# Optimization experiments

Measured on AMD Instinct MI355X. Metric: run time of the kernel, lower is better.

Reference implementation:

```python
import jax, jax.numpy as jnp
import numpy as np

B, S, D, H = 4, 2048, 512, 8
DH = D // H  # 64


def setup_inputs() -> dict:
    key = jax.random.key(0)
    ks = jax.random.split(key, 12)
    sc = 0.02
    return {
        "embed": jax.random.normal(ks[0], (B, S, D), dtype=jnp.float32),
        "Wq": jax.random.normal(ks[1], (H, DH, D), dtype=jnp.float32) * sc,
        "bq": jax.random.normal(ks[2], (H, DH), dtype=jnp.float32) * sc,
        "Wk": jax.random.normal(ks[3], (H, DH, D), dtype=jnp.float32) * sc,
        "bk": jax.random.normal(ks[4], (H, DH), dtype=jnp.float32) * sc,
        "Wv": jax.random.normal(ks[5], (H, DH, D), dtype=jnp.float32) * sc,
        "bv": jax.random.normal(ks[6], (H, DH), dtype=jnp.float32) * sc,
        "Wo": jax.random.normal(ks[7], (D, D), dtype=jnp.float32) * sc,
        "bo": jax.random.normal(ks[8], (D,), dtype=jnp.float32) * sc,
        "gamma": jnp.ones((D,), dtype=jnp.float32),
        "beta": jnp.zeros((D,), dtype=jnp.float32),
    }


def reference(embed, Wq, bq, Wk, bk, Wv, bv, Wo, bo, gamma, beta):
    # Per-head linear projections, vectorized over heads: [B,H,S,DH]
    q = jnp.einsum("bsd,hed->bhse", embed, Wq) + bq[None, :, None, :]
    k = jnp.einsum("bsd,hed->bhse", embed, Wk) + bk[None, :, None, :]
    v = jnp.einsum("bsd,hed->bhse", embed, Wv) + bv[None, :, None, :]

    # Full score matrix [B,H,S,S], tril applied to RAW scores (zeros, not -inf),
    # scaled by sqrt(embedding_dim) -- faithful to the original module's math.
    att = jnp.einsum("bhse,bhte->bhst", q, k)
    att = jnp.tril(att)
    att = att / jnp.sqrt(jnp.float32(D))
    att = jax.nn.softmax(att, axis=-1)

    out = jnp.einsum("bhst,bhte->bhse", att, v)  # [B,H,S,DH]
    # concat heads along feature dim -> [B,S,D]
    out = jnp.transpose(out, (0, 2, 1, 3)).reshape(B, S, D)

    x = out @ Wo.T + bo
    x = x + embed

    # LayerNorm over last dim
    mu = jnp.mean(x, axis=-1, keepdims=True)
    var = jnp.var(x, axis=-1, keepdims=True)
    x = (x - mu) / jnp.sqrt(var + 1e-5) * gamma + beta
    return x
```

## Files before the change

### kernel.cpp

```cpp
#include <hip/hip_runtime.h>
#include <hip/hip_bf16.h>


typedef __bf16 bf16;
typedef __bf16 bf16x8 __attribute__((ext_vector_type(8)));
typedef __bf16 bf16x4v __attribute__((ext_vector_type(4)));
typedef float f32x4 __attribute__((ext_vector_type(4)));

#define S_LEN 2048
#define DMODEL 512
#define QSCALE 0.06375870914f

#define GLDS(g, l) __builtin_amdgcn_global_load_lds(                  \
    (const __attribute__((address_space(1))) void*)(g),               \
    (__attribute__((address_space(3))) void*)(l), 16, 0, 0)

#define EXP2(x) __builtin_amdgcn_exp2f(x)

__global__ __launch_bounds__(256) void cast_all(
    const float* __restrict__ embed, const float* __restrict__ Wq,
    const float* __restrict__ Wk, const float* __restrict__ Wv,
    const float* __restrict__ Wo,
    bf16* __restrict__ Eb, bf16* __restrict__ Wqkv, bf16* __restrict__ Wob) {
  int i = blockIdx.x * 256 + threadIdx.x;
  const float* src;
  bf16* dst;
  int il;
  if (i < 1048576) {
    src = embed; dst = Eb; il = i;
  } else {
    int j = i - 1048576;
    int w = j >> 16;
    il = j & 65535;
    src = (w == 0) ? Wq : (w == 1) ? Wk : (w == 2) ? Wv : Wo;
    dst = (w == 3) ? Wob : Wqkv + (size_t)w * 262144;
  }
  float4 v = reinterpret_cast<const float4*>(src)[il];
  bf16x4v o;
  o[0] = (bf16)v.x; o[1] = (bf16)v.y; o[2] = (bf16)v.z; o[3] = (bf16)v.w;
  *reinterpret_cast<bf16x4v*>(dst + (size_t)il * 4) = o;
}

__device__ __forceinline__ void gemm128_core(
    const bf16* __restrict__ A, const bf16* __restrict__ Bw,
    int row0, int col0, bf16* As, bf16* Bs, f32x4 (&acc)[4][4]) {
  int tid = threadIdx.x;
  int w = tid >> 6, l = tid & 63, lr = l & 15, lg = l >> 4;
  int wr = w >> 1, wc = w & 1;

  int srow = w * 8 + (l >> 3);
  int scol = ((l & 7) ^ (srow & 7)) << 3;
  const bf16* ga = A + (size_t)(row0 + srow) * DMODEL + scol;
  const bf16* gb = Bw + (size_t)(col0 + srow) * DMODEL + scol;
  char* asb = (char*)As;
  char* bsb = (char*)Bs;
  int sbase = w * 1024;

  int aoff[4], boff[4];
#pragma unroll
  for (int m = 0; m < 4; ++m) {
    aoff[m] = (wr * 64 + m * 16 + lr) * 128 + (((lg ^ (lr & 7))) << 4);
    boff[m] = (wc * 64 + m * 16 + lr) * 128 + (((lg ^ (lr & 7))) << 4);
  }

  for (int k0 = 0; k0 < DMODEL; k0 += 64) {
#pragma unroll
    for (int qt = 0; qt < 4; ++qt) {
      GLDS(ga + (size_t)qt * 32 * DMODEL, asb + qt * 4096 + sbase);
      GLDS(gb + (size_t)qt * 32 * DMODEL, bsb + qt * 4096 + sbase);
    }
    ga += 64; gb += 64;
    __syncthreads();

    bf16x8 af[2][4], bfv[2][4];
#pragma unroll
    for (int m = 0; m < 4; ++m) {
      af[0][m] = *(const bf16x8*)(asb + aoff[m]);
      af[1][m] = *(const bf16x8*)(asb + (aoff[m] ^ 0x40));
      bfv[0][m] = *(const bf16x8*)(bsb + boff[m]);
      bfv[1][m] = *(const bf16x8*)(bsb + (boff[m] ^ 0x40));
    }
#pragma unroll
    for (int m = 0; m < 4; ++m)
#pragma unroll
      for (int n = 0; n < 4; ++n) {
        acc[m][n] = __builtin_amdgcn_mfma_f32_16x16x32_bf16(af[0][m], bfv[0][n], acc[m][n], 0, 0, 0);
        acc[m][n] = __builtin_amdgcn_mfma_f32_16x16x32_bf16(af[1][m], bfv[1][n], acc[m][n], 0, 0, 0);
      }
    __syncthreads();
  }
}

__global__ __launch_bounds__(256) void gemm_qkv(
    const bf16* __restrict__ A, const bf16* __restrict__ Wqkv,
    const float* __restrict__ bq, const float* __restrict__ bk, const float* __restrict__ bv,
    bf16* __restrict__ Qb, bf16* __restrict__ Kb, bf16* __restrict__ Vt) {
  __shared__ __align__(16) bf16 As[128 * 64];
  __shared__ __align__(16) bf16 Bs[128 * 64];
  int row0 = blockIdx.x * 128, col0 = blockIdx.y * 128;
  f32x4 acc[4][4] = {};
  gemm128_core(A, Wqkv, row0, col0, As, Bs, acc);

  int tid = threadIdx.x;
  int w = tid >> 6, l = tid & 63, lr = l & 15, lg = l >> 4;
  int wr = w >> 1, wc = w & 1;
  int z2 = col0 >> 9;
  if (z2 < 2) {
    bf16* O = z2 ? Kb : Qb;
    const float* bias = z2 ? bk : bq;
    float qs = z2 ? 1.0f : QSCALE;
#pragma unroll
    for (int n = 0; n < 4; ++n) {
      int cg = (col0 & 511) + wc * 64 + n * 16 + lr;
      float bi = bias[cg];
#pragma unroll
      for (int m = 0; m < 4; ++m) {
        int rg = row0 + wr * 64 + m * 16 + lg * 4;
#pragma unroll
        for (int r = 0; r < 4; ++r)
          O[(size_t)(rg + r) * DMODEL + cg] = (bf16)((acc[m][n][r] + bi) * qs);
      }
    }
  } else {
#pragma unroll
    for (int n = 0; n < 4; ++n) {
      int ep = (col0 & 511) + wc * 64 + n * 16 + lr;
      int h = ep >> 6, e = ep & 63;
      float bi = bv[ep];
#pragma unroll
      for (int m = 0; m < 4; ++m) {
        int rg = row0 + wr * 64 + m * 16 + lg * 4;
        int b = rg >> 11, s0 = rg & 2047;
        bf16x4v pk;
#pragma unroll
        for (int r = 0; r < 4; ++r) pk[r] = (bf16)(acc[m][n][r] + bi);
        *(bf16x4v*)(Vt + ((size_t)((b * 8 + h) * 64 + e)) * S_LEN + s0) = pk;
      }
    }
  }
}

__global__ __launch_bounds__(256) void gemm_wo(
    const bf16* __restrict__ A, const bf16* __restrict__ W,
    const float* __restrict__ bo, const float* __restrict__ embed,
    bf16* __restrict__ X) {
  __shared__ __align__(16) bf16 As[128 * 64];
  __shared__ __align__(16) bf16 Bs[128 * 64];
  int row0 = blockIdx.x * 128, col0 = blockIdx.y * 128;
  f32x4 acc[4][4] = {};
  gemm128_core(A, W, row0, col0, As, Bs, acc);

  int tid = threadIdx.x;
  int w = tid >> 6, l = tid & 63, lr = l & 15, lg = l >> 4;
  int wr = w >> 1, wc = w & 1;
#pragma unroll
  for (int n = 0; n < 4; ++n) {
    int cg = col0 + wc * 64 + n * 16 + lr;
    float bi = bo[cg];
#pragma unroll
    for (int m = 0; m < 4; ++m) {
      int rg = row0 + wr * 64 + m * 16 + lg * 4;
#pragma unroll
      for (int r = 0; r < 4; ++r)
        X[(size_t)(rg + r) * DMODEL + cg] =
            (bf16)(acc[m][n][r] + bi + embed[(size_t)(rg + r) * DMODEL + cg]);
    }
  }
}

__global__ __launch_bounds__(256) void suf_kernel(const bf16* __restrict__ Vt,
                                                  float* __restrict__ SUF) {
  int bh = blockIdx.x >> 3;
  int eg = blockIdx.x & 7;
  int el = threadIdx.x & 7;
  int seg = threadIdx.x >> 3;
  int e = eg * 8 + el;
  __shared__ float segtot[32][9];
  const bf16* vrow = Vt + ((size_t)bh * 64 + e) * S_LEN;
  float loc[4];
  float carry = 0.f;
#pragma unroll
  for (int j = 3; j >= 0; --j) {
    int jj = seg * 4 + j;
    bf16x8 a = *(const bf16x8*)(vrow + jj * 16);
    bf16x8 b2 = *(const bf16x8*)(vrow + jj * 16 + 8);
    float s = 0.f;
#pragma unroll
    for (int k = 0; k < 8; ++k) s += (float)a[k] + (float)b2[k];
    carry += s;
    loc[j] = carry;
  }
  segtot[seg][el] = carry;
  __syncthreads();
  float add = 0.f;
  for (int s2 = seg + 1; s2 < 32; ++s2) add += segtot[s2][el];
  float* srow = SUF + (size_t)bh * 129 * 64 + e;
#pragma unroll
  for (int j = 0; j < 4; ++j) srow[(size_t)(seg * 4 + j) * 64] = loc[j] + add;
  if (seg == 0) srow[(size_t)128 * 64] = 0.f;
}

__global__ __launch_bounds__(512) void flash_attn(
    const bf16* __restrict__ Qb, const bf16* __restrict__ Kb,
    const bf16* __restrict__ Vt, const float* __restrict__ SUF,
    bf16* __restrict__ attO) {
  int id = blockIdx.x;
  int g = id & 7;
  int j = id >> 3;
  int bh = g * 4 + (j & 3);
  int p = 15 - (j >> 2);
  int b = bh >> 3, h = bh & 7;
  int tid = threadIdx.x;
  int w = tid >> 6, l = tid & 63, lr = l & 15, lg = l >> 4;
  int wsub = w & 3;
  int qtile = (w < 4) ? (16 + p) : (15 - p);
  int qb = qtile * 64;
  int qbw = qb + 16 * wsub;
  int tmax_w = qbw + 16;
  int nt = (18 + p) >> 1;
  int ntw = (tmax_w + 127) >> 7;

  __shared__ __align__(16) bf16 kl[2][128 * 64];
  __shared__ __align__(16) bf16 vl[2][2][64 * 64];
  __shared__ __align__(16) bf16 pl[8][16 * 64];

  const bf16* qptr = Qb + ((size_t)(b * S_LEN) + qbw + lr) * DMODEL + h * 64 + lg * 8;
  bf16x8 aq0 = *(const bf16x8*)(qptr);
  bf16x8 aq1 = *(const bf16x8*)(qptr + 32);

  float lsum[4] = {0.f, 0.f, 0.f, 0.f};
  f32x4 acc[4] = {};

  int grow = tid >> 3, gch = tid & 7;
  int sch = ((gch ^ (grow & 7)) << 3);
  const bf16* Kg = Kb + ((size_t)(b * S_LEN) + grow) * DMODEL + h * 64 + sch;
  const bf16* Vg = Vt + ((size_t)(bh * 64) + grow) * S_LEN + sch;
  int sdst = w * 1024;

  int sw0 = (lg ^ (lr & 7)) << 4;
  int sw4 = sw0 ^ 0x40;
  char* plb = (char*)pl[w];

  GLDS(Kg, (char*)kl[0] + sdst);
  GLDS(Kg + (size_t)64 * DMODEL, (char*)kl[0] + 8192 + sdst);
  GLDS(Vg, (char*)vl[0][0] + sdst);
  GLDS(Vg + 64, (char*)vl[0][1] + sdst);
  asm volatile("s_waitcnt vmcnt(0)" ::: "memory");
  __syncthreads();

  int cur = 0;
  for (int it = 0; it < nt; ++it) {
    int t0 = it << 7;
    if (it + 1 < nt) {
      GLDS(Kg + (size_t)(t0 + 128) * DMODEL, (char*)kl[cur ^ 1] + sdst);
      GLDS(Kg + (size_t)(t0 + 192) * DMODEL, (char*)kl[cur ^ 1] + 8192 + sdst);
      GLDS(Vg + (t0 + 128), (char*)vl[cur ^ 1][0] + sdst);
      GLDS(Vg + (t0 + 192), (char*)vl[cur ^ 1][1] + sdst);
    }
    if (it < ntw) {
      char* klb = (char*)kl[cur];
      bool ph1 = (t0 + 64) < tmax_w;

      f32x4 sf[8];
      const f32x4 fz = {0.f, 0.f, 0.f, 0.f};
      int ncq = ph1 ? 8 : 4;
      __builtin_amdgcn_s_setprio(1);
#pragma unroll 8
      for (int c = 0; c < 8; ++c) {
        if (c < ncq) {
          int rb = (16 * c + lr) * 128;
          bf16x8 bk0 = *(const bf16x8*)(klb + rb + sw0);
          bf16x8 bk1 = *(const bf16x8*)(klb + rb + sw4);
          f32x4 t = __builtin_amdgcn_mfma_f32_16x16x32_bf16(aq0, bk0, fz, 0, 0, 0);
          sf[c] = __builtin_amdgcn_mfma_f32_16x16x32_bf16(aq1, bk1, t, 0, 0, 0);
        }
      }
      __builtin_amdgcn_s_setprio(0);

#pragma unroll
      for (int hp = 0; hp < 2; ++hp) {
        int t0p = t0 + 64 * hp;
        if (hp == 1 && !ph1) break;
        char* vlb = (char*)vl[cur][hp];

        if (t0p + 64 <= qbw) {
#pragma unroll
          for (int r = 0; r < 4; ++r) {
            int row = lg * 4 + r;
            int pbase = row * 128 + ((lr & 7) << 1);
            int xorv = row & 7;
            float psum = 0.f;
#pragma unroll
            for (int c = 0; c < 4; ++c) {
              float pv = EXP2(sf[4 * hp + c][r]);
              psum += pv;
              int chunk = 2 * c + (lr >> 3);
              *(bf16*)(plb + pbase + (((chunk ^ xorv) << 4))) = (bf16)pv;
            }
            lsum[r] += psum;
          }
        } else {
#pragma unroll
          for (int r = 0; r < 4; ++r) {
            int sg = qbw + lg * 4 + r;
            int row = lg * 4 + r;
            int pbase = row * 128 + ((lr & 7) << 1);
            int xorv = row & 7;
            float psum = 0.f;
#pragma unroll
            for (int c = 0; c < 4; ++c) {
              int tg = t0p + 16 * c + lr;
              float x = (tg <= sg) ? sf[4 * hp + c][r] : ((tg < tmax_w) ? 0.f : -1e30f);
              float pv = EXP2(x);
              psum += pv;
              int chunk = 2 * c + (lr >> 3);
              *(bf16*)(plb + pbase + (((chunk ^ xorv) << 4))) = (bf16)pv;
            }
            lsum[r] += psum;
          }
        }

        bf16x8 pa0 = *(const bf16x8*)(plb + lr * 128 + sw0);
        bf16x8 pa1 = *(const bf16x8*)(plb + lr * 128 + sw4);
        __builtin_amdgcn_s_setprio(1);
#pragma unroll
        for (int c = 0; c < 4; ++c) {
          int rb = (16 * c + lr) * 128;
          bf16x8 bv0 = *(const bf16x8*)(vlb + rb + sw0);
          bf16x8 bv1 = *(const bf16x8*)(vlb + rb + sw4);
          acc[c] = __builtin_amdgcn_mfma_f32_16x16x32_bf16(pa0, bv0, acc[c], 0, 0, 0);
          acc[c] = __builtin_amdgcn_mfma_f32_16x16x32_bf16(pa1, bv1, acc[c], 0, 0, 0);
        }
        __builtin_amdgcn_s_setprio(0);
      }
    }
    asm volatile("s_waitcnt vmcnt(0)" ::: "memory");
    __syncthreads();
    cur ^= 1;
  }

#pragma unroll
  for (int r = 0; r < 4; ++r) {
#pragma unroll
    for (int d = 1; d < 16; d <<= 1) lsum[r] += __shfl_xor(lsum[r], d, 64);
  }

  int j16 = tmax_w >> 4;
  const float* suf = SUF + ((size_t)bh * 129 + j16) * 64;
  float cnt = (float)(S_LEN - tmax_w);
  float sufe[4];
#pragma unroll
  for (int c = 0; c < 4; ++c) sufe[c] = suf[16 * c + lr];
#pragma unroll
  for (int r = 0; r < 4; ++r) {
    float inv = 1.f / (lsum[r] + cnt);
    int sg = qbw + lg * 4 + r;
#pragma unroll
    for (int c = 0; c < 4; ++c) {
      float o = (acc[c][r] + sufe[c]) * inv;
      attO[((size_t)(b * S_LEN) + sg) * DMODEL + h * 64 + 16 * c + lr] = (bf16)o;
    }
  }
}

__global__ __launch_bounds__(256) void ln_kernel(const bf16* __restrict__ x,
                                                 const float* __restrict__ gamma,
                                                 const float* __restrict__ beta,
                                                 float* __restrict__ out) {
  int row = blockIdx.x * 4 + (threadIdx.x >> 6);
  int l = threadIdx.x & 63;
  bf16x8 xv = *(const bf16x8*)(x + (size_t)row * DMODEL + l * 8);
  float xf[8];
  float s = 0.f, s2 = 0.f;
#pragma unroll
  for (int k = 0; k < 8; ++k) {
    xf[k] = (float)xv[k];
    s += xf[k];
    s2 += xf[k] * xf[k];
  }
#pragma unroll
  for (int d = 1; d < 64; d <<= 1) {
    s += __shfl_xor(s, d, 64);
    s2 += __shfl_xor(s2, d, 64);
  }
  float mean = s * (1.f / 512.f);
  float var = s2 * (1.f / 512.f) - mean * mean;
  float rstd = rsqrtf(var + 1e-5f);
  const float4* g4 = reinterpret_cast<const float4*>(gamma) + l * 2;
  const float4* b4 = reinterpret_cast<const float4*>(beta) + l * 2;
  float4 g0 = g4[0], g1 = g4[1], bb0 = b4[0], bb1 = b4[1];
  float4 o0, o1;
  o0.x = (xf[0] - mean) * rstd * g0.x + bb0.x;
  o0.y = (xf[1] - mean) * rstd * g0.y + bb0.y;
  o0.z = (xf[2] - mean) * rstd * g0.z + bb0.z;
  o0.w = (xf[3] - mean) * rstd * g0.w + bb0.w;
  o1.x = (xf[4] - mean) * rstd * g1.x + bb1.x;
  o1.y = (xf[5] - mean) * rstd * g1.y + bb1.y;
  o1.z = (xf[6] - mean) * rstd * g1.z + bb1.z;
  o1.w = (xf[7] - mean) * rstd * g1.w + bb1.w;
  float4* orow = reinterpret_cast<float4*>(out + (size_t)row * DMODEL) + l * 2;
  orow[0] = o0;
  orow[1] = o1;
}

extern "C" void kernel_launch(void* const* d_in, const int* in_sizes, int n_in,
                              void* d_out, int out_size, void* d_ws, size_t ws_size,
                              hipStream_t stream) {
  const float* embed = (const float*)d_in[0];
  const float* Wq = (const float*)d_in[1];
  const float* bq = (const float*)d_in[2];
  const float* Wk = (const float*)d_in[3];
  const float* bk = (const float*)d_in[4];
  const float* Wv = (const float*)d_in[5];
  const float* bv = (const float*)d_in[6];
  const float* Wo = (const float*)d_in[7];
  const float* bo = (const float*)d_in[8];
  const float* gamma = (const float*)d_in[9];
  const float* beta = (const float*)d_in[10];
  float* out = (float*)d_out;

  char* ws = (char*)d_ws;
  size_t off = 0;
  auto alc = [&](size_t b) { size_t o = off; off += (b + 255) & ~(size_t)255; return o; };
  bf16* Eb    = (bf16*)(ws + alc(8192ull * 512 * 2));
  bf16* Wqkv  = (bf16*)(ws + alc(1536ull * 512 * 2));
  bf16* Wob   = (bf16*)(ws + alc(512ull * 512 * 2));
  bf16* Qb    = (bf16*)(ws + alc(8192ull * 512 * 2));
  bf16* Kb    = (bf16*)(ws + alc(8192ull * 512 * 2));
  bf16* Vt    = (bf16*)(ws + alc(8192ull * 512 * 2));
  float* SUF  = (float*)(ws + alc(32ull * 129 * 64 * 4));
  bf16* AttO  = (bf16*)(ws + alc(8192ull * 512 * 2));
  bf16* Xb    = (bf16*)(ws + alc(8192ull * 512 * 2));
  (void)ws_size; (void)n_in; (void)in_sizes; (void)out_size;

  cast_all<<<5120, 256, 0, stream>>>(embed, Wq, Wk, Wv, Wo, Eb, Wqkv, Wob);

  gemm_qkv<<<dim3(64, 12), 256, 0, stream>>>(Eb, Wqkv, bq, bk, bv, Qb, Kb, Vt);
  suf_kernel<<<256, 256, 0, stream>>>(Vt, SUF);
  flash_attn<<<512, 512, 0, stream>>>(Qb, Kb, Vt, SUF, AttO);
  gemm_wo<<<dim3(64, 4), 256, 0, stream>>>(AttO, Wob, bo, embed, Xb);
  ln_kernel<<<2048, 256, 0, stream>>>(Xb, gamma, beta, out);
}
```

Measured before the change: 92.06 us.

## Double-buffer GEMM K-loop with BK=32 and prefetch next tile

Reworks the shared 128x128 GEMM core from single-buffered BK=64 tiles to double-buffered BK=32 tiles. The next K slice is loaded via global_load_lds while MFMAs run on the current buffer, aiming to hide global load latency. The XOR swizzle is dropped, so LDS reads use a plain row stride of 64 bytes, which risks bank conflicts. It also takes twice as many barrier and waitcnt iterations.

New measurement: 92.55 us. About the same (+0.5%).

```diff
diff --git a/kernel.cpp b/kernel.cpp
--- a/kernel.cpp
+++ b/kernel.cpp
@@ -48,45 +48,54 @@
   int w = tid >> 6, l = tid & 63, lr = l & 15, lg = l >> 4;
   int wr = w >> 1, wc = w & 1;
 
-  int srow = w * 8 + (l >> 3);
-  int scol = ((l & 7) ^ (srow & 7)) << 3;
-  const bf16* ga = A + (size_t)(row0 + srow) * DMODEL + scol;
-  const bf16* gb = Bw + (size_t)(col0 + srow) * DMODEL + scol;
+  int srow = w * 16 + (l >> 2);
+  int sk = (l & 3) * 8;
+  const bf16* ga = A + (size_t)(row0 + srow) * DMODEL + sk;
+  const bf16* gb = Bw + (size_t)(col0 + srow) * DMODEL + sk;
   char* asb = (char*)As;
   char* bsb = (char*)Bs;
-  int sbase = w * 1024;
+  int sdst = w * 1024;
 
   int aoff[4], boff[4];
 #pragma unroll
   for (int m = 0; m < 4; ++m) {
-    aoff[m] = (wr * 64 + m * 16 + lr) * 128 + (((lg ^ (lr & 7))) << 4);
-    boff[m] = (wc * 64 + m * 16 + lr) * 128 + (((lg ^ (lr & 7))) << 4);
-  }
-
-  for (int k0 = 0; k0 < DMODEL; k0 += 64) {
-#pragma unroll
-    for (int qt = 0; qt < 4; ++qt) {
-      GLDS(ga + (size_t)qt * 32 * DMODEL, asb + qt * 4096 + sbase);
-      GLDS(gb + (size_t)qt * 32 * DMODEL, bsb + qt * 4096 + sbase);
-    }
-    ga += 64; gb += 64;
-    __syncthreads();
-
-    bf16x8 af[2][4], bfv[2][4];
+    aoff[m] = (wr * 64 + m * 16 + lr) * 64 + lg * 16;
+    boff[m] = (wc * 64 + m * 16 + lr) * 64 + lg * 16;
+  }
+
+  GLDS(ga, asb + sdst);
+  GLDS(ga + (size_t)64 * DMODEL, asb + 4096 + sdst);
+  GLDS(gb, bsb + sdst);
+  GLDS(gb + (size_t)64 * DMODEL, bsb + 4096 + sdst);
+  asm volatile("s_waitcnt vmcnt(0)" ::: "memory");
+  __syncthreads();
+
+#pragma unroll
+  for (int kk = 0; kk < 16; ++kk) {
+    int cur = kk & 1;
+    if (kk + 1 < 16) {
+      int kn = (kk + 1) * 32;
+      char* an = asb + (cur ^ 1) * 8192 + sdst;
+      char* bn = bsb + (cur ^ 1) * 8192 + sdst;
+      GLDS(ga + kn, an);
+      GLDS(ga + (size_t)64 * DMODEL + kn, an + 4096);
+      GLDS(gb + kn, bn);
+      GLDS(gb + (size_t)64 * DMODEL + kn, bn + 4096);
+    }
+    char* ab = asb + cur * 8192;
+    char* bb = bsb + cur * 8192;
+    bf16x8 af[4], bfv[4];
 #pragma unroll
     for (int m = 0; m < 4; ++m) {
-      af[0][m] = *(const bf16x8*)(asb + aoff[m]);
-      af[1][m] = *(const bf16x8*)(asb + (aoff[m] ^ 0x40));
-      bfv[0][m] = *(const bf16x8*)(bsb + boff[m]);
-      bfv[1][m] = *(const bf16x8*)(bsb + (boff[m] ^ 0x40));
+      af[m] = *(const bf16x8*)(ab + aoff[m]);
+      bfv[m] = *(const bf16x8*)(bb + boff[m]);
     }
 #pragma unroll
     for (int m = 0; m < 4; ++m)
 #pragma unroll
-      for (int n = 0; n < 4; ++n) {
-        acc[m][n] = __builtin_amdgcn_mfma_f32_16x16x32_bf16(af[0][m], bfv[0][n], acc[m][n], 0, 0, 0);
-        acc[m][n] = __builtin_amdgcn_mfma_f32_16x16x32_bf16(af[1][m], bfv[1][n], acc[m][n], 0, 0, 0);
-      }
+      for (int n = 0; n < 4; ++n)
+        acc[m][n] = __builtin_amdgcn_mfma_f32_16x16x32_bf16(af[m], bfv[n], acc[m][n], 0, 0, 0);
+    asm volatile("s_waitcnt vmcnt(0)" ::: "memory");
     __syncthreads();
   }
 }
@@ -95,8 +104,8 @@
     const bf16* __restrict__ A, const bf16* __restrict__ Wqkv,
     const float* __restrict__ bq, const float* __restrict__ bk, const float* __restrict__ bv,
     bf16* __restrict__ Qb, bf16* __restrict__ Kb, bf16* __restrict__ Vt) {
-  __shared__ __align__(16) bf16 As[128 * 64];
-  __shared__ __align__(16) bf16 Bs[128 * 64];
+  __shared__ __align__(16) bf16 As[2 * 128 * 32];
+  __shared__ __align__(16) bf16 Bs[2 * 128 * 32];
   int row0 = blockIdx.x * 128, col0 = blockIdx.y * 128;
   f32x4 acc[4][4] = {};
   gemm128_core(A, Wqkv, row0, col0, As, Bs, acc);
@@ -144,8 +153,8 @@
     const bf16* __restrict__ A, const bf16* __restrict__ W,
     const float* __restrict__ bo, const float* __restrict__ embed,
     bf16* __restrict__ X) {
-  __shared__ __align__(16) bf16 As[128 * 64];
-  __shared__ __align__(16) bf16 Bs[128 * 64];
+  __shared__ __align__(16) bf16 As[2 * 128 * 32];
+  __shared__ __align__(16) bf16 Bs[2 * 128 * 32];
   int row0 = blockIdx.x * 128, col0 = blockIdx.y * 128;
   f32x4 acc[4][4] = {};
   gemm128_core(A, W, row0, col0, As, Bs, acc);
```
